# Kernel optimization log

Measured on AMD Instinct MI355X. Metric: run time of the kernel, lower is better.

The kernel has to match this reference:

```python
import jax, jax.numpy as jnp
import numpy as np

C = 1024
HEADS = 8
HD = C // HEADS
SF = 2
EPS = 1e-6
N, D, H, W = 2, 32, 40, 32


def _ln(x, w, b):
    m = jnp.mean(x, -1, keepdims=True)
    v = jnp.mean((x - m) ** 2, -1, keepdims=True)
    return (x - m) * jax.lax.rsqrt(v + EPS) * w + b


def _mlp2(x, w1, b1, w2, b2):
    # Linear -> exact GELU -> Linear (matches nn.Sequential(Linear, GELU, Linear))
    return jax.nn.gelu(x @ w1.T + b1, approximate=False) @ w2.T + b2


def setup_inputs() -> dict:
    key = jax.random.key(0)
    ks = jax.random.split(key, 24)
    p = lambda i, shape: jax.random.normal(ks[i], shape, jnp.float32) * 0.02
    return {
        "x": jax.random.normal(ks[0], (N, D, H, W, C), jnp.float32),
        "q_w": p(1, (C, C)),
        "k_w1": p(2, (C, C)), "k_b1": p(3, (C,)),
        "k_w2": p(4, (C, C)), "k_b2": p(5, (C,)),
        "v_w1": p(6, (C, C)), "v_b1": p(7, (C,)),
        "v_w2": p(8, (C, C)), "v_b2": p(9, (C,)),
        "lnq_w": jnp.ones((C,), jnp.float32), "lnq_b": jnp.zeros((C,), jnp.float32),
        "lnk_w": jnp.ones((C,), jnp.float32), "lnk_b": jnp.zeros((C,), jnp.float32),
        "lnv_w": jnp.ones((C,), jnp.float32), "lnv_b": jnp.zeros((C,), jnp.float32),
        "in_w": p(10, (3 * C, C)), "in_b": p(11, (3 * C,)),
        "out_w": p(12, (C, C)), "out_b": p(13, (C,)),
        "mlp_w1": p(14, (2 * C, C)), "mlp_b1": p(15, (2 * C,)),
        "mlp_w2": p(16, (2 * C, 2 * C)), "mlp_b2": p(17, (2 * C,)),
    }


def reference(x, q_w, k_w1, k_b1, k_w2, k_b2, v_w1, v_b1, v_w2, v_b2,
              lnq_w, lnq_b, lnk_w, lnk_b, lnv_w, lnv_b,
              in_w, in_b, out_w, out_b, mlp_w1, mlp_b1, mlp_w2, mlp_b2):
    n, d, h, w, c = x.shape
    dg, hg, wg = d // SF, h // SF, w // SF
    cube = SF ** 3

    x_flat = x.reshape(n, -1, c)                      # [N, T, C], T = D*H*W
    k = _ln(_mlp2(x_flat, k_w1, k_b1, k_w2, k_b2), lnk_w, lnk_b)
    v = _ln(_mlp2(x_flat, v_w1, v_b1, v_w2, v_b2), lnv_w, lnv_b)

    # Trilinear downsample by exactly 2 (align_corners=False) == 2x2x2 mean pool.
    q = x.reshape(n, dg, SF, hg, SF, wg, SF, c).mean(axis=(2, 4, 6))
    q = q.reshape(n, -1, c)                            # [N, Q, C]
    query = _ln(q @ q_w.T, lnq_w, lnq_b)               # q_proj_1 has no bias

    def regions(t):
        t = t.reshape(n, dg, SF, hg, SF, wg, SF, c)
        t = t.transpose(0, 1, 3, 5, 2, 4, 6, 7)
        return t.reshape(n, dg * hg * wg, cube, c)     # [N, Q, 8, C]

    k_r = regions(k)
    v_r = regions(v)

    wq, wk, wv = in_w[:C], in_w[C:2 * C], in_w[2 * C:]
    bq, bk, bv = in_b[:C], in_b[C:2 * C], in_b[2 * C:]
    qh = (query @ wq.T + bq).reshape(n, -1, HEADS, HD)           # [N,Q,h,hd]
    kh = (k_r @ wk.T + bk).reshape(n, -1, cube, HEADS, HD)       # [N,Q,8,h,hd]
    vh = (v_r @ wv.T + bv).reshape(n, -1, cube, HEADS, HD)

    scale = 1.0 / np.sqrt(HD).astype(np.float32)
    scores = jnp.einsum('nqhd,nqkhd->nqhk', qh, kh) * scale
    attn = jax.nn.softmax(scores, axis=-1)
    o = jnp.einsum('nqhk,nqkhd->nqhd', attn, vh).reshape(n, -1, c)
    o = o @ out_w.T + out_b                            # MHA out_proj

    o = _mlp2(o, mlp_w1, mlp_b1, mlp_w2, mlp_b2)       # [N, Q, 2C]
    return o.reshape(n, dg, hg, wg, 2 * c)
```

## Files before the change

kernel.cpp:

```cpp
#include <hip/hip_runtime.h>

typedef __attribute__((ext_vector_type(8))) short bf16x8;
typedef __attribute__((ext_vector_type(4))) float f32x4;
typedef unsigned short u16;

__device__ inline u16 f2b(float f) {
  union { float f; unsigned u; } x; x.f = f;
  unsigned r = x.u + 0x7FFFu + ((x.u >> 16) & 1u);
  return (u16)(r >> 16);
}
__device__ inline float b2f(u16 s) {
  union { unsigned u; float f; } x; x.u = ((unsigned)s) << 16;
  return x.f;
}
__device__ inline float gelu_f(float v) {
  return 0.5f * v * (1.0f + erff(v * 0.70710678118654752f));
}
__device__ inline void gll16(const void* g, void* lds) {
  __builtin_amdgcn_global_load_lds((const __attribute__((address_space(1))) void*)g,
                                   (__attribute__((address_space(3))) void*)lds,
                                   16, 0, 0);
}

__global__ __launch_bounds__(256) void cvt_w(const float* __restrict__ s,
                                             u16* __restrict__ d, int n4) {
  int i = blockIdx.x * 256 + threadIdx.x;
  if (i < n4) {
    float4 v = ((const float4*)s)[i];
    ushort4 o; o.x = f2b(v.x); o.y = f2b(v.y); o.z = f2b(v.z); o.w = f2b(v.w);
    ((ushort4*)d)[i] = o;
  }
}

__global__ __launch_bounds__(256) void cat_bias(const float* __restrict__ a,
                                                const float* __restrict__ b,
                                                float* __restrict__ o) {
  int i = blockIdx.x * 256 + threadIdx.x;
  if (i < 1024) { o[i] = a[i]; o[1024 + i] = b[i]; }
}

__global__ __launch_bounds__(256) void pool_cvt(const float* __restrict__ xg,
                                                u16* __restrict__ Xb,
                                                u16* __restrict__ Qp) {
  int qr = blockIdx.x;
  int wgi = qr & 15;
  int hgi = (qr >> 4) % 20;
  int dgi = qr / 320;
  int c = threadIdx.x * 4;
  float sx = 0.f, sy = 0.f, sz = 0.f, sw = 0.f;
#pragma unroll
  for (int j = 0; j < 8; ++j) {
    int tr = ((2 * dgi + (j >> 2)) * 40 + (2 * hgi + ((j >> 1) & 1))) * 32 +
             (2 * wgi + (j & 1));
    long off = (long)tr * 1024 + c;
    float4 v = *(const float4*)&xg[off];
    ushort4 o; o.x = f2b(v.x); o.y = f2b(v.y); o.z = f2b(v.z); o.w = f2b(v.w);
    *(ushort4*)&Xb[off] = o;
    sx += v.x; sy += v.y; sz += v.z; sw += v.w;
  }
  ushort4 o;
  o.x = f2b(sx * 0.125f); o.y = f2b(sy * 0.125f);
  o.z = f2b(sz * 0.125f); o.w = f2b(sw * 0.125f);
  *(ushort4*)&Qp[(long)qr * 1024 + c] = o;
}

__global__ __launch_bounds__(256) void ln_ip(u16* __restrict__ X,
                                             const float* __restrict__ w,
                                             const float* __restrict__ b) {
  long row = blockIdx.x;
  int c = threadIdx.x * 4;
  ushort4 v = *(const ushort4*)&X[row * 1024 + c];
  float f0 = b2f(v.x), f1 = b2f(v.y), f2 = b2f(v.z), f3 = b2f(v.w);
  float s = f0 + f1 + f2 + f3;
  float q = f0 * f0 + f1 * f1 + f2 * f2 + f3 * f3;
#pragma unroll
  for (int off = 32; off >= 1; off >>= 1) {
    s += __shfl_xor(s, off);
    q += __shfl_xor(q, off);
  }
  __shared__ float red[8];
  int wv = threadIdx.x >> 6, ln = threadIdx.x & 63;
  if (ln == 0) { red[wv] = s; red[4 + wv] = q; }
  __syncthreads();
  s = red[0] + red[1] + red[2] + red[3];
  q = red[4] + red[5] + red[6] + red[7];
  float mean = s * (1.f / 1024.f);
  float var = q * (1.f / 1024.f) - mean * mean;
  float rs = rsqrtf(var + 1e-6f);
  float4 wv4 = *(const float4*)&w[c];
  float4 bv4 = *(const float4*)&b[c];
  ushort4 o;
  o.x = f2b((f0 - mean) * rs * wv4.x + bv4.x);
  o.y = f2b((f1 - mean) * rs * wv4.y + bv4.y);
  o.z = f2b((f2 - mean) * rs * wv4.z + bv4.z);
  o.w = f2b((f3 - mean) * rs * wv4.w + bv4.w);
  *(ushort4*)&X[row * 1024 + c] = o;
}

#define HALF 8192
#define MFMA16(a, b, c) __builtin_amdgcn_mfma_f32_16x16x32_bf16((a), (b), (c), 0, 0, 0)

template <int EPI>
__global__ __launch_bounds__(512, 2) void gemm256(const u16* __restrict__ A,
                                                  const u16* __restrict__ B,
                                                  const float* __restrict__ bias,
                                                  float* __restrict__ Cf,
                                                  u16* __restrict__ Cb,
                                                  int M, int N, int K, int lda,
                                                  int nbx, int nby) {
  extern __shared__ u16 lds[];
  u16* ASm = lds;
  u16* BSm = lds + 4 * HALF;
  const int tid = threadIdx.x;
  const int l = tid & 63, w = tid >> 6;
  const int wr = w >> 2, wc = w & 3;
  const int lr = l & 15, kg = l >> 4;
  const int e7 = l & 7;

  int L = blockIdx.x, bx, by;
  if ((nbx & 7) == 0) {
    int xcd = L & 7, j = L >> 3, ppx = nbx >> 3;
    int pj = j / nby;
    bx = xcd * ppx + pj;
    by = j - pj * nby;
  } else {
    bx = L % nbx;
    by = L / nbx;
  }
  const int bm = bx * 256, bn = by * 256;

  const int c0 = w * 64 + l, c1 = 512 + c0;
  const int r0 = c0 >> 3, cs0 = (c0 & 7) ^ (r0 & 7);
  const int r1 = c1 >> 3, cs1 = (c1 & 7) ^ (r1 & 7);
  const u16* Ab = A + (long)bm * lda;
  const u16* Bb = B + (long)bn * K;
  int a0r0 = min(bm + r0, M - 1) - bm;
  int a0r1 = min(bm + r1, M - 1) - bm;
  int a1r0 = min(bm + 128 + r0, M - 1) - bm;
  int a1r1 = min(bm + 128 + r1, M - 1) - bm;
  const int oA00 = a0r0 * lda + cs0 * 8, oA01 = a0r1 * lda + cs1 * 8;
  const int oA10 = a1r0 * lda + cs0 * 8, oA11 = a1r1 * lda + cs1 * 8;
  const int oB00 = r0 * K + cs0 * 8, oB01 = r1 * K + cs1 * 8;
  const int oB10 = (128 + r0) * K + cs0 * 8, oB11 = (128 + r1) * K + cs1 * 8;
  const int d0 = c0 * 8, d1 = c1 * 8;

  const int sw0 = ((kg) ^ e7) * 8;
  const int sw1 = ((4 + kg) ^ e7) * 8;

  f32x4 acc[8][4] = {};
  bf16x8 af[4][2], bf[2][2][2];
  const int nt = K / 64;

#define STG_A(slot, o0_, o1_, ko) do { \
    gll16(Ab + (o0_) + (ko), ASm + (slot) * HALF + d0); \
    gll16(Ab + (o1_) + (ko), ASm + (slot) * HALF + d1); } while (0)
#define STG_B(slot, o0_, o1_, ko) do { \
    gll16(Bb + (o0_) + (ko), BSm + (slot) * HALF + d0); \
    gll16(Bb + (o1_) + (ko), BSm + (slot) * HALF + d1); } while (0)

  STG_A(0, oA00, oA01, 0); STG_A(1, oA10, oA11, 0);
  STG_B(0, oB00, oB01, 0); STG_B(1, oB10, oB11, 0);
  STG_A(2, oA00, oA01, 64); STG_B(2, oB00, oB01, 64); STG_B(3, oB10, oB11, 64);
  asm volatile("s_waitcnt vmcnt(6)" ::: "memory");
  __builtin_amdgcn_s_barrier();

  const int rbA = wr * 64 + lr;
  const int rbB = (wc & 1) * 64 + lr;

  for (int t = 0; t < nt; ++t) {
    const int p = t & 1, qp = p ^ 1;
    const int kn1 = (t + 1 < nt ? t + 1 : nt - 1) * 64;
    const int kn2 = (t + 2 < nt ? t + 2 : nt - 1) * 64;
    const u16* sa0 = ASm + (p * 2 + 0) * HALF;
    const u16* sa1 = ASm + (p * 2 + 1) * HALF;
    const u16* sb = BSm + (p * 2 + (wc >> 1)) * HALF;

#pragma unroll
    for (int mq = 0; mq < 4; ++mq) {
      af[mq][0] = *(const bf16x8*)&sa0[(rbA + mq * 16) * 64 + sw0];
      af[mq][1] = *(const bf16x8*)&sa0[(rbA + mq * 16) * 64 + sw1];
    }
#pragma unroll
    for (int nn = 0; nn < 2; ++nn) {
      bf[0][nn][0] = *(const bf16x8*)&sb[(rbB + nn * 16) * 64 + sw0];
      bf[0][nn][1] = *(const bf16x8*)&sb[(rbB + nn * 16) * 64 + sw1];
    }
    STG_A(qp * 2 + 1, oA10, oA11, kn1);
    __builtin_amdgcn_s_barrier();
    __builtin_amdgcn_s_setprio(1);
#pragma unroll
    for (int mq = 0; mq < 4; ++mq)
#pragma unroll
      for (int nn = 0; nn < 2; ++nn) {
        acc[mq][nn] = MFMA16(af[mq][0], bf[0][nn][0], acc[mq][nn]);
        acc[mq][nn] = MFMA16(af[mq][1], bf[0][nn][1], acc[mq][nn]);
      }
    __builtin_amdgcn_s_setprio(0);
    __builtin_amdgcn_s_barrier();

#pragma unroll
    for (int nn = 0; nn < 2; ++nn) {
      bf[1][nn][0] = *(const bf16x8*)&sb[(rbB + (2 + nn) * 16) * 64 + sw0];
      bf[1][nn][1] = *(const bf16x8*)&sb[(rbB + (2 + nn) * 16) * 64 + sw1];
    }
    STG_A(p * 2 + 0, oA00, oA01, kn2);
    __builtin_amdgcn_s_barrier();
    __builtin_amdgcn_s_setprio(1);
#pragma unroll
    for (int mq = 0; mq < 4; ++mq)
#pragma unroll
      for (int nn = 0; nn < 2; ++nn) {
        acc[mq][2 + nn] = MFMA16(af[mq][0], bf[1][nn][0], acc[mq][2 + nn]);
        acc[mq][2 + nn] = MFMA16(af[mq][1], bf[1][nn][1], acc[mq][2 + nn]);
      }
    __builtin_amdgcn_s_setprio(0);
    __builtin_amdgcn_s_barrier();

#pragma unroll
    for (int mq = 0; mq < 4; ++mq) {
      af[mq][0] = *(const bf16x8*)&sa1[(rbA + mq * 16) * 64 + sw0];
      af[mq][1] = *(const bf16x8*)&sa1[(rbA + mq * 16) * 64 + sw1];
    }
    STG_B(p * 2 + 0, oB00, oB01, kn2);
    __builtin_amdgcn_s_barrier();
    __builtin_amdgcn_s_setprio(1);
#pragma unroll
    for (int mq = 0; mq < 4; ++mq)
#pragma unroll
      for (int nn = 0; nn < 2; ++nn) {
        acc[4 + mq][nn] = MFMA16(af[mq][0], bf[0][nn][0], acc[4 + mq][nn]);
        acc[4 + mq][nn] = MFMA16(af[mq][1], bf[0][nn][1], acc[4 + mq][nn]);
      }
    __builtin_amdgcn_s_setprio(0);
    __builtin_amdgcn_s_barrier();

    STG_B(p * 2 + 1, oB10, oB11, kn2);
    asm volatile("s_waitcnt vmcnt(6)" ::: "memory");
    __builtin_amdgcn_s_barrier();
    __builtin_amdgcn_s_setprio(1);
#pragma unroll
    for (int mq = 0; mq < 4; ++mq)
#pragma unroll
      for (int nn = 0; nn < 2; ++nn) {
        acc[4 + mq][2 + nn] = MFMA16(af[mq][0], bf[1][nn][0], acc[4 + mq][2 + nn]);
        acc[4 + mq][2 + nn] = MFMA16(af[mq][1], bf[1][nn][1], acc[4 + mq][2 + nn]);
      }
    __builtin_amdgcn_s_setprio(0);
    __builtin_amdgcn_s_barrier();
  }
  asm volatile("s_waitcnt vmcnt(0)" ::: "memory");
#undef STG_A
#undef STG_B

#pragma unroll
  for (int m = 0; m < 8; ++m) {
    int row = bm + (m >> 2) * 128 + wr * 64 + (m & 3) * 16 + kg * 4;
#pragma unroll
    for (int n = 0; n < 4; ++n) {
      int col = bn + wc * 64 + n * 16 + lr;
      float bsv = (EPI == 3) ? 0.f : bias[col];
#pragma unroll
      for (int r = 0; r < 4; ++r) {
        if (row + r < M) {
          float v = acc[m][n][r] + bsv;
          if (EPI == 1) v = gelu_f(v);
          if (EPI == 2) Cf[(long)(row + r) * N + col] = v;
          else Cb[(long)(row + r) * N + col] = f2b(v);
        }
      }
    }
  }
}

__global__ __launch_bounds__(256) void attn_k(const u16* __restrict__ QH,
                                              const u16* __restrict__ KH,
                                              const u16* __restrict__ VH,
                                              u16* __restrict__ O) {
  int qr = blockIdx.x;
  int wgi = qr & 15;
  int hgi = (qr >> 4) % 20;
  int dgi = qr / 320;
  int c0 = (threadIdx.x >> 5) * 128 + (threadIdx.x & 31) * 4;
  ushort4 qv = *(const ushort4*)&QH[(long)qr * 1024 + c0];
  float q0 = b2f(qv.x), q1 = b2f(qv.y), q2 = b2f(qv.z), q3 = b2f(qv.w);
  long trs[8];
  float sc[8];
#pragma unroll
  for (int j = 0; j < 8; ++j) {
    int tr = ((2 * dgi + (j >> 2)) * 40 + (2 * hgi + ((j >> 1) & 1))) * 32 +
             (2 * wgi + (j & 1));
    trs[j] = (long)tr * 1024 + c0;
    ushort4 kv = *(const ushort4*)&KH[trs[j]];
    float p = q0 * b2f(kv.x) + q1 * b2f(kv.y) + q2 * b2f(kv.z) + q3 * b2f(kv.w);
    p += __shfl_xor(p, 16); p += __shfl_xor(p, 8); p += __shfl_xor(p, 4);
    p += __shfl_xor(p, 2);  p += __shfl_xor(p, 1);
    sc[j] = p * 0.088388347648318447f;
  }
  float mx = sc[0];
#pragma unroll
  for (int j = 1; j < 8; ++j) mx = fmaxf(mx, sc[j]);
  float ssum = 0.f;
#pragma unroll
  for (int j = 0; j < 8; ++j) { sc[j] = expf(sc[j] - mx); ssum += sc[j]; }
  float inv = 1.0f / ssum;
  float o0 = 0, o1 = 0, o2 = 0, o3 = 0;
#pragma unroll
  for (int j = 0; j < 8; ++j) {
    ushort4 vv = *(const ushort4*)&VH[trs[j]];
    float p = sc[j] * inv;
    o0 += p * b2f(vv.x); o1 += p * b2f(vv.y);
    o2 += p * b2f(vv.z); o3 += p * b2f(vv.w);
  }
  ushort4 ov; ov.x = f2b(o0); ov.y = f2b(o1); ov.z = f2b(o2); ov.w = f2b(o3);
  *(ushort4*)&O[(long)qr * 1024 + c0] = ov;
}

extern "C" void kernel_launch(void* const* d_in, const int* in_sizes, int n_in,
                              void* d_out, int out_size, void* d_ws,
                              size_t ws_size, hipStream_t stream) {
  const float* x      = (const float*)d_in[0];
  const float* q_w    = (const float*)d_in[1];
  const float* k_w1   = (const float*)d_in[2];
  const float* k_b1   = (const float*)d_in[3];
  const float* k_w2   = (const float*)d_in[4];
  const float* k_b2   = (const float*)d_in[5];
  const float* v_w1   = (const float*)d_in[6];
  const float* v_b1   = (const float*)d_in[7];
  const float* v_w2   = (const float*)d_in[8];
  const float* v_b2   = (const float*)d_in[9];
  const float* lnq_w  = (const float*)d_in[10];
  const float* lnq_b  = (const float*)d_in[11];
  const float* lnk_w  = (const float*)d_in[12];
  const float* lnk_b  = (const float*)d_in[13];
  const float* lnv_w  = (const float*)d_in[14];
  const float* lnv_b  = (const float*)d_in[15];
  const float* in_w   = (const float*)d_in[16];
  const float* in_b   = (const float*)d_in[17];
  const float* out_w  = (const float*)d_in[18];
  const float* out_b  = (const float*)d_in[19];
  const float* mlp_w1 = (const float*)d_in[20];
  const float* mlp_b1 = (const float*)d_in[21];
  const float* mlp_w2 = (const float*)d_in[22];
  const float* mlp_b2 = (const float*)d_in[23];
  float* out = (float*)d_out;

  hipFuncSetAttribute((const void*)gemm256<0>, hipFuncAttributeMaxDynamicSharedMemorySize, 131072);
  hipFuncSetAttribute((const void*)gemm256<1>, hipFuncAttributeMaxDynamicSharedMemorySize, 131072);
  hipFuncSetAttribute((const void*)gemm256<2>, hipFuncAttributeMaxDynamicSharedMemorySize, 131072);
  hipFuncSetAttribute((const void*)gemm256<3>, hipFuncAttributeMaxDynamicSharedMemorySize, 131072);

  char* base = (char*)d_ws;
  size_t off = 0;
  auto alloc_us = [&](size_t elems) -> u16* {
    u16* r = (u16*)(base + off);
    off += ((elems * 2 + 255) & ~(size_t)255);
    return r;
  };
  const size_t CC = 1024 * 1024;
  u16* wb_q   = alloc_us(CC);
  u16* wb_kv1 = alloc_us(2 * CC);
  u16* wb_k2  = alloc_us(CC);
  u16* wb_v2  = alloc_us(CC);
  u16* wb_in  = alloc_us(3 * CC);
  u16* wb_out = alloc_us(CC);
  u16* wb_m1  = alloc_us(2 * CC);
  u16* wb_m2  = alloc_us(4 * CC);
  float* b_kv1 = (float*)(base + off); off += 2048 * 4;

  auto cvt = [&](const float* s, u16* d, size_t n) {
    int n4 = (int)(n / 4);
    cvt_w<<<(n4 + 255) / 256, 256, 0, stream>>>(s, d, n4);
  };
  cvt(q_w, wb_q, CC);
  cvt(k_w1, wb_kv1, CC);        cvt(v_w1, wb_kv1 + CC, CC);
  cvt(k_w2, wb_k2, CC);         cvt(v_w2, wb_v2, CC);
  cvt(in_w, wb_in, 3 * CC);     cvt(out_w, wb_out, CC);
  cvt(mlp_w1, wb_m1, 2 * CC);   cvt(mlp_w2, wb_m2, 4 * CC);
  cat_bias<<<4, 256, 0, stream>>>(k_b1, v_b1, b_kv1);

  int s = 16;
  for (int cand = 1; cand <= 16; cand <<= 1) {
    size_t Tc_ = 40960ull / cand;
    size_t need = off + Tc_ * 11520ull + (1ull << 20);
    if (need <= ws_size) { s = cand; break; }
  }
  const int dcount = 32 / s;
  const int dgc = dcount / 2;
  const int Tc = dcount * 1280;
  const int Tq = dgc * 320;

  u16* Xb  = alloc_us((size_t)Tc * 1024);
  u16* Hb2 = alloc_us((size_t)Tc * 2048);
  u16* Kb  = alloc_us((size_t)Tc * 1024);
  u16* Vb  = alloc_us((size_t)Tc * 1024);
  u16* Qp  = alloc_us((size_t)Tq * 1024);
  u16* QQ  = alloc_us((size_t)Tq * 1024);
  u16* QHb = alloc_us((size_t)Tq * 1024);
  u16* Ob  = alloc_us((size_t)Tq * 1024);
  u16* O2  = alloc_us((size_t)Tq * 1024);
  u16* Hm  = Kb;

  auto launch_gemm = [&](int EPI, const u16* A, const u16* B, const float* bias,
                         float* Cf, u16* Cb, int M, int N, int K, int lda) {
    int nbx = (M + 255) / 256, nby = N / 256;
    dim3 g(nbx * nby);
    switch (EPI) {
      case 0: gemm256<0><<<g, 512, 131072, stream>>>(A, B, bias, Cf, Cb, M, N, K, lda, nbx, nby); break;
      case 1: gemm256<1><<<g, 512, 131072, stream>>>(A, B, bias, Cf, Cb, M, N, K, lda, nbx, nby); break;
      case 2: gemm256<2><<<g, 512, 131072, stream>>>(A, B, bias, Cf, Cb, M, N, K, lda, nbx, nby); break;
      default: gemm256<3><<<g, 512, 131072, stream>>>(A, B, bias, Cf, Cb, M, N, K, lda, nbx, nby); break;
    }
  };

  for (int n = 0; n < 2; ++n) {
    for (int sl = 0; sl < s; ++sl) {
      long tok0 = (long)n * 40960 + (long)sl * dcount * 1280;
      long q0g  = (long)n * 5120 + (long)sl * dgc * 320;
      const float* xg = x + tok0 * 1024;

      pool_cvt<<<Tq, 256, 0, stream>>>(xg, Xb, Qp);

      launch_gemm(1, Xb, wb_kv1, b_kv1, nullptr, Hb2, Tc, 2048, 1024, 1024);
      launch_gemm(0, Hb2, wb_k2, k_b2, nullptr, Kb, Tc, 1024, 1024, 2048);
      ln_ip<<<Tc, 256, 0, stream>>>(Kb, lnk_w, lnk_b);
      launch_gemm(0, Hb2 + 1024, wb_v2, v_b2, nullptr, Vb, Tc, 1024, 1024, 2048);
      ln_ip<<<Tc, 256, 0, stream>>>(Vb, lnv_w, lnv_b);

      launch_gemm(3, Qp, wb_q, nullptr, nullptr, QQ, Tq, 1024, 1024, 1024);
      ln_ip<<<Tq, 256, 0, stream>>>(QQ, lnq_w, lnq_b);
      launch_gemm(0, QQ, wb_in, in_b, nullptr, QHb, Tq, 1024, 1024, 1024);

      launch_gemm(0, Kb, wb_in + CC, in_b + 1024, nullptr, Xb, Tc, 1024, 1024, 1024);
      launch_gemm(0, Vb, wb_in + 2 * CC, in_b + 2048, nullptr, Hb2, Tc, 1024, 1024, 1024);

      attn_k<<<Tq, 256, 0, stream>>>(QHb, Xb, Hb2, Ob);

      launch_gemm(0, Ob, wb_out, out_b, nullptr, O2, Tq, 1024, 1024, 1024);
      launch_gemm(1, O2, wb_m1, mlp_b1, nullptr, Hm, Tq, 2048, 1024, 1024);
      launch_gemm(2, Hm, wb_m2, mlp_b2, out + q0g * 2048, nullptr, Tq, 2048, 2048, 2048);
    }
  }
}
```

Measured before the change: 2.685 ms.

## Group paired K/V GEMMs into one launch and add 128-tile GEMM for small shapes

The K and V second-layer GEMMs, and the K and V in-projection GEMMs, are each merged into a single grouped launch. Blocks past the first M rows switch to the second operand set, which doubles the grid and reduces launch count and tail waves. A new 128x128 double-buffered GEMM handles small or non-256-aligned shapes (the Tq-sized query, out-proj and MLP GEMMs) to improve occupancy on under-filled grids. The vmcnt wait threshold in the 256 kernel also changes, which risks a load/compute ordering hazard if it is wrong for the number of outstanding loads.

Measured after the change: 2.450 ms. 1.1x faster.

```diff
diff --git a/kernel.cpp b/kernel.cpp
--- a/kernel.cpp
+++ b/kernel.cpp
@@ -97,25 +97,22 @@
   *(ushort4*)&X[row * 1024 + c] = o;
 }
 
-#define HALF 8192
 #define MFMA16(a, b, c) __builtin_amdgcn_mfma_f32_16x16x32_bf16((a), (b), (c), 0, 0, 0)
 
+#define BK 32
 template <int EPI>
-__global__ __launch_bounds__(512, 2) void gemm256(const u16* __restrict__ A,
-                                                  const u16* __restrict__ B,
-                                                  const float* __restrict__ bias,
-                                                  float* __restrict__ Cf,
-                                                  u16* __restrict__ Cb,
-                                                  int M, int N, int K, int lda,
-                                                  int nbx, int nby) {
-  extern __shared__ u16 lds[];
-  u16* ASm = lds;
-  u16* BSm = lds + 4 * HALF;
+__global__ __launch_bounds__(256) void gemm_bt(const u16* __restrict__ A,
+                                               const u16* __restrict__ B,
+                                               const float* __restrict__ bias,
+                                               float* __restrict__ Cf,
+                                               u16* __restrict__ Cb,
+                                               int M, int N, int K, int lda,
+                                               int nbx, int nby) {
+  __shared__ __align__(16) u16 As0[128 * BK];
+  __shared__ __align__(16) u16 Bs0[128 * BK];
+  __shared__ __align__(16) u16 As1[128 * BK];
+  __shared__ __align__(16) u16 Bs1[128 * BK];
   const int tid = threadIdx.x;
-  const int l = tid & 63, w = tid >> 6;
-  const int wr = w >> 2, wc = w & 3;
-  const int lr = l & 15, kg = l >> 4;
-  const int e7 = l & 7;
 
   int L = blockIdx.x, bx, by;
   if ((nbx & 7) == 0) {
@@ -127,7 +124,119 @@
     bx = L % nbx;
     by = L / nbx;
   }
-  const int bm = bx * 256, bn = by * 256;
+  const int bm = bx * 128, bn = by * 128;
+
+  const int l = tid & 63, wv = tid >> 6;
+  const int wm = (wv >> 1) * 64, wn = (wv & 1) * 64;
+  const int lr = l & 15, kg = l >> 4;
+
+  const int ea = tid * 8, eb = (256 + tid) * 8;
+  const int ra = ea >> 5, ca = ea & 31;
+  const int rb = eb >> 5, cbn = eb & 31;
+  int gra = bm + ra; if (gra > M - 1) gra = M - 1;
+  int grb = bm + rb; if (grb > M - 1) grb = M - 1;
+  const u16* pa0 = A + (long)gra * lda + ca;
+  const u16* pa1 = A + (long)grb * lda + cbn;
+  const u16* pb0 = B + (long)(bn + ra) * K + ca;
+  const u16* pb1 = B + (long)(bn + rb) * K + cbn;
+
+  f32x4 acc[4][4] = {};
+  const int nt = K / BK;
+
+#define STAGE(AS, BS, k0)                \
+  do {                                   \
+    gll16(pa0 + (k0), &(AS)[ea]);        \
+    gll16(pb0 + (k0), &(BS)[ea]);        \
+    gll16(pa1 + (k0), &(AS)[eb]);        \
+    gll16(pb1 + (k0), &(BS)[eb]);        \
+  } while (0)
+
+#define COMPUTE(AS, BS)                                                       \
+  do {                                                                        \
+    bf16x8 af[4], bfr[4];                                                     \
+    _Pragma("unroll") for (int m = 0; m < 4; ++m)                             \
+        af[m] = *(const bf16x8*)&(AS)[(wm + m * 16 + lr) * BK + kg * 8];      \
+    _Pragma("unroll") for (int n = 0; n < 4; ++n)                             \
+        bfr[n] = *(const bf16x8*)&(BS)[(wn + n * 16 + lr) * BK + kg * 8];     \
+    _Pragma("unroll") for (int m = 0; m < 4; ++m)                             \
+        _Pragma("unroll") for (int n = 0; n < 4; ++n)                         \
+            acc[m][n] = MFMA16(af[m], bfr[n], acc[m][n]);                     \
+  } while (0)
+
+  STAGE(As0, Bs0, 0);
+  __syncthreads();
+  for (int t = 0; t < nt; t += 2) {
+    if (t + 1 < nt) STAGE(As1, Bs1, (t + 1) * BK);
+    COMPUTE(As0, Bs0);
+    __syncthreads();
+    if (t + 2 < nt) STAGE(As0, Bs0, (t + 2) * BK);
+    COMPUTE(As1, Bs1);
+    __syncthreads();
+  }
+#undef STAGE
+#undef COMPUTE
+
+#pragma unroll
+  for (int m = 0; m < 4; ++m) {
+    int row0 = bm + wm + m * 16 + kg * 4;
+#pragma unroll
+    for (int n = 0; n < 4; ++n) {
+      int col = bn + wn + n * 16 + lr;
+      float bsv = (EPI == 3) ? 0.f : bias[col];
+#pragma unroll
+      for (int r = 0; r < 4; ++r) {
+        int row = row0 + r;
+        if (row < M) {
+          float v = acc[m][n][r] + bsv;
+          if (EPI == 1) v = gelu_f(v);
+          if (EPI == 2) Cf[(long)row * N + col] = v;
+          else Cb[(long)row * N + col] = f2b(v);
+        }
+      }
+    }
+  }
+}
+
+#define HALF 8192
+template <int EPI>
+__global__ __launch_bounds__(512, 2) void g256(const u16* __restrict__ A,
+                                               const u16* __restrict__ B,
+                                               const float* __restrict__ bias,
+                                               float* __restrict__ Cf,
+                                               u16* __restrict__ Cb,
+                                               int M1, int N, int K, int lda,
+                                               int nbx, int nby,
+                                               const u16* __restrict__ A2,
+                                               const u16* __restrict__ B2,
+                                               const float* __restrict__ bias2,
+                                               u16* __restrict__ Cb2, int M2) {
+  extern __shared__ u16 lds[];
+  u16* ASm = lds;
+  u16* BSm = lds + 4 * HALF;
+  const int tid = threadIdx.x;
+  const int l = tid & 63, w = tid >> 6;
+  const int wr = w >> 2, wc = w & 3;
+  const int lr = l & 15, kg = l >> 4;
+  const int e7 = l & 7;
+
+  int L = blockIdx.x, bx, by;
+  if ((nbx & 7) == 0) {
+    int xcd = L & 7, j = L >> 3, ppx = nbx >> 3;
+    int pj = j / nby;
+    bx = xcd * ppx + pj;
+    by = j - pj * nby;
+  } else {
+    bx = L % nbx;
+    by = L / nbx;
+  }
+  int bm = bx * 256;
+  const int bn = by * 256;
+
+  int M = M1;
+  if (bm >= M1) {
+    A = A2; B = B2; bias = bias2; Cb = Cb2;
+    bm -= M1; M = M2;
+  }
 
   const int c0 = w * 64 + l, c1 = 512 + c0;
   const int r0 = c0 >> 3, cs0 = (c0 & 7) ^ (r0 & 7);
@@ -235,7 +344,7 @@
     __builtin_amdgcn_s_barrier();
 
     STG_B(p * 2 + 1, oB10, oB11, kn2);
-    asm volatile("s_waitcnt vmcnt(6)" ::: "memory");
+    asm volatile("s_waitcnt vmcnt(8)" ::: "memory");
     __builtin_amdgcn_s_barrier();
     __builtin_amdgcn_s_setprio(1);
 #pragma unroll
@@ -344,10 +453,10 @@
   const float* mlp_b2 = (const float*)d_in[23];
   float* out = (float*)d_out;
 
-  hipFuncSetAttribute((const void*)gemm256<0>, hipFuncAttributeMaxDynamicSharedMemorySize, 131072);
-  hipFuncSetAttribute((const void*)gemm256<1>, hipFuncAttributeMaxDynamicSharedMemorySize, 131072);
-  hipFuncSetAttribute((const void*)gemm256<2>, hipFuncAttributeMaxDynamicSharedMemorySize, 131072);
-  hipFuncSetAttribute((const void*)gemm256<3>, hipFuncAttributeMaxDynamicSharedMemorySize, 131072);
+  hipFuncSetAttribute((const void*)g256<0>, hipFuncAttributeMaxDynamicSharedMemorySize, 131072);
+  hipFuncSetAttribute((const void*)g256<1>, hipFuncAttributeMaxDynamicSharedMemorySize, 131072);
+  hipFuncSetAttribute((const void*)g256<2>, hipFuncAttributeMaxDynamicSharedMemorySize, 131072);
+  hipFuncSetAttribute((const void*)g256<3>, hipFuncAttributeMaxDynamicSharedMemorySize, 131072);
 
   char* base = (char*)d_ws;
   size_t off = 0;
@@ -400,15 +509,35 @@
   u16* O2  = alloc_us((size_t)Tq * 1024);
   u16* Hm  = Kb;
 
+  auto launch_g256_grp = [&](int EPI, const u16* A1, const u16* B1,
+                             const float* bias1, float* Cf, u16* Cb1, int M1,
+                             const u16* A2, const u16* B2, const float* bias2,
+                             u16* Cb2, int M2, int N, int K, int lda) {
+    int nbx = (M1 + M2) / 256, nby = N / 256;
+    dim3 g(nbx * nby);
+    switch (EPI) {
+      case 0: g256<0><<<g, 512, 131072, stream>>>(A1, B1, bias1, Cf, Cb1, M1, N, K, lda, nbx, nby, A2, B2, bias2, Cb2, M2); break;
+      case 1: g256<1><<<g, 512, 131072, stream>>>(A1, B1, bias1, Cf, Cb1, M1, N, K, lda, nbx, nby, A2, B2, bias2, Cb2, M2); break;
+      case 2: g256<2><<<g, 512, 131072, stream>>>(A1, B1, bias1, Cf, Cb1, M1, N, K, lda, nbx, nby, A2, B2, bias2, Cb2, M2); break;
+      default: g256<3><<<g, 512, 131072, stream>>>(A1, B1, bias1, Cf, Cb1, M1, N, K, lda, nbx, nby, A2, B2, bias2, Cb2, M2); break;
+    }
+  };
+
   auto launch_gemm = [&](int EPI, const u16* A, const u16* B, const float* bias,
                          float* Cf, u16* Cb, int M, int N, int K, int lda) {
-    int nbx = (M + 255) / 256, nby = N / 256;
-    dim3 g(nbx * nby);
-    switch (EPI) {
-      case 0: gemm256<0><<<g, 512, 131072, stream>>>(A, B, bias, Cf, Cb, M, N, K, lda, nbx, nby); break;
-      case 1: gemm256<1><<<g, 512, 131072, stream>>>(A, B, bias, Cf, Cb, M, N, K, lda, nbx, nby); break;
-      case 2: gemm256<2><<<g, 512, 131072, stream>>>(A, B, bias, Cf, Cb, M, N, K, lda, nbx, nby); break;
-      default: gemm256<3><<<g, 512, 131072, stream>>>(A, B, bias, Cf, Cb, M, N, K, lda, nbx, nby); break;
+    int b256 = (M / 256) * (N / 256);
+    if ((M % 256) == 0 && (N % 256) == 0 && b256 >= 256) {
+      launch_g256_grp(EPI, A, B, bias, Cf, Cb, M, nullptr, nullptr, nullptr,
+                      nullptr, 0, N, K, lda);
+    } else {
+      int nbx = (M + 127) / 128, nby = N / 128;
+      dim3 g(nbx * nby);
+      switch (EPI) {
+        case 0: gemm_bt<0><<<g, 256, 0, stream>>>(A, B, bias, Cf, Cb, M, N, K, lda, nbx, nby); break;
+        case 1: gemm_bt<1><<<g, 256, 0, stream>>>(A, B, bias, Cf, Cb, M, N, K, lda, nbx, nby); break;
+        case 2: gemm_bt<2><<<g, 256, 0, stream>>>(A, B, bias, Cf, Cb, M, N, K, lda, nbx, nby); break;
+        default: gemm_bt<3><<<g, 256, 0, stream>>>(A, B, bias, Cf, Cb, M, N, K, lda, nbx, nby); break;
+      }
     }
   };
 
@@ -421,17 +550,17 @@
       pool_cvt<<<Tq, 256, 0, stream>>>(xg, Xb, Qp);
 
       launch_gemm(1, Xb, wb_kv1, b_kv1, nullptr, Hb2, Tc, 2048, 1024, 1024);
-      launch_gemm(0, Hb2, wb_k2, k_b2, nullptr, Kb, Tc, 1024, 1024, 2048);
+      launch_g256_grp(0, Hb2, wb_k2, k_b2, nullptr, Kb, Tc,
+                      Hb2 + 1024, wb_v2, v_b2, Vb, Tc, 1024, 1024, 2048);
       ln_ip<<<Tc, 256, 0, stream>>>(Kb, lnk_w, lnk_b);
-      launch_gemm(0, Hb2 + 1024, wb_v2, v_b2, nullptr, Vb, Tc, 1024, 1024, 2048);
       ln_ip<<<Tc, 256, 0, stream>>>(Vb, lnv_w, lnv_b);
 
       launch_gemm(3, Qp, wb_q, nullptr, nullptr, QQ, Tq, 1024, 1024, 1024);
       ln_ip<<<Tq, 256, 0, stream>>>(QQ, lnq_w, lnq_b);
       launch_gemm(0, QQ, wb_in, in_b, nullptr, QHb, Tq, 1024, 1024, 1024);
 
-      launch_gemm(0, Kb, wb_in + CC, in_b + 1024, nullptr, Xb, Tc, 1024, 1024, 1024);
-      launch_gemm(0, Vb, wb_in + 2 * CC, in_b + 2048, nullptr, Hb2, Tc, 1024, 1024, 1024);
+      launch_g256_grp(0, Kb, wb_in + CC, in_b + 1024, nullptr, Xb, Tc,
+                      Vb, wb_in + 2 * CC, in_b + 2048, Hb2, Tc, 1024, 1024, 1024);
 
       attn_k<<<Tq, 256, 0, stream>>>(QHb, Xb, Hb2, Ob);
 
```
